# Kernel optimization log

Measured on AMD Instinct MI355X. Metric: run time of the kernel, lower is better.

## Reference

```python
import jax, jax.numpy as jnp
import numpy as np
import math

H = 256      # hidden_dim
L = 2        # num_layers
K = 30       # prediction_length
TD = 32      # time_encoding_dim
DT = 0.1


def _time_encodings():
    # (K, TD): sinusoidal PE over TD-1 dims + normalized time ratio, per _get_time_encoding
    pos = jnp.arange(K, dtype=jnp.float32)[:, None]
    div = jnp.exp(jnp.arange(0, TD - 1, 2, dtype=jnp.float32) * (-math.log(10000.0) / (TD - 1)))
    pe = jnp.zeros((K, TD - 1), dtype=jnp.float32)
    pe = pe.at[:, 0::2].set(jnp.sin(pos * div))
    pe = pe.at[:, 1::2].set(jnp.cos(pos * div[: (TD - 1) // 2]))
    return jnp.concatenate([pe, pos / K], axis=1)


def _gru_cell(x, h, Wih, Whh, bih, bhh):
    # PyTorch GRU cell: r,z,n gate order
    gi = x @ Wih.T + bih
    gh = h @ Whh.T + bhh
    ir, iz, inn = jnp.split(gi, 3, axis=1)
    hr, hz, hn = jnp.split(gh, 3, axis=1)
    r = jax.nn.sigmoid(ir + hr)
    z = jax.nn.sigmoid(iz + hz)
    n = jnp.tanh(inn + r * hn)
    return (1.0 - z) * n + z * h


def setup_inputs() -> dict:
    key = jax.random.key(0)
    ks = jax.random.split(key, 16)
    B = 4096
    in0 = 3 + TD + H  # gru_input_size = 291
    s = 0.05
    p = lambda k, shp: jax.random.normal(k, shp, dtype=jnp.float32) * s
    return {
        'h_fused': jax.random.normal(ks[0], (B, H), dtype=jnp.float32),
        'initial_state': jax.random.normal(ks[1], (B, 3), dtype=jnp.float32),
        'W1': p(ks[2], (H, H)), 'b1': jnp.zeros((H,), jnp.float32),
        'W2': p(ks[3], (L * H, H)), 'b2': jnp.zeros((L * H,), jnp.float32),
        'Wih0': p(ks[4], (3 * H, in0)), 'Whh0': p(ks[5], (3 * H, H)),
        'bih0': jnp.zeros((3 * H,), jnp.float32), 'bhh0': jnp.zeros((3 * H,), jnp.float32),
        'Wih1': p(ks[6], (3 * H, H)), 'Whh1': p(ks[7], (3 * H, H)),
        'bih1': jnp.zeros((3 * H,), jnp.float32), 'bhh1': jnp.zeros((3 * H,), jnp.float32),
        'Wout': p(ks[8], (3, H)), 'bout': jnp.zeros((3,), jnp.float32),
    }


def reference(h_fused, initial_state, W1, b1, W2, b2,
              Wih0, Whh0, bih0, bhh0, Wih1, Whh1, bih1, bhh1, Wout, bout):
    B = h_fused.shape[0]
    # init_mlp: Linear -> ReLU -> Linear -> Tanh, reshape to per-layer hidden states
    h_init = jnp.tanh(jax.nn.relu(h_fused @ W1.T + b1) @ W2.T + b2)  # (B, L*H)
    h_layers = h_init.reshape(B, L, H).transpose(1, 0, 2)            # (L, B, H)
    te = _time_encodings()                                           # (K, TD)
    pos0 = jnp.repeat(initial_state[:, 0:1], 3, axis=1)              # position history window

    def step(carry, te_k):
        s_t, h0, h1, pos_hist = carry
        gin = jnp.concatenate([s_t, jnp.broadcast_to(te_k, (B, TD)), h_fused], axis=1)
        h0n = _gru_cell(gin, h0, Wih0, Whh0, bih0, bhh0)
        h1n = _gru_cell(h0n, h1, Wih1, Whh1, bih1, bhh1)
        qr = h1n @ Wout.T + bout                                     # (B, 3)
        q_lo = qr[:, 0]
        q_med = q_lo + jax.nn.softplus(qr[:, 1] - q_lo)
        q_hi = q_med + jax.nn.softplus(qr[:, 2] - q_med)
        x_next = q_med  # inference path (no teacher forcing)
        ph = jnp.concatenate([pos_hist[:, 1:], x_next[:, None]], axis=1)
        v = (ph[:, 2] - ph[:, 0]) / (2.0 * DT)                       # central-diff velocity
        a = (ph[:, 2] - 2.0 * ph[:, 1] + ph[:, 0]) / (DT * DT)       # second-diff accel
        s_next = jnp.stack([x_next, v, a], axis=1)
        return (s_next, h0n, h1n, ph), (q_lo, q_med, q_hi)

    _, (qlo, qmed, qhi) = jax.lax.scan(step, (initial_state, h_layers[0], h_layers[1], pos0), te)
    # scan stacks along step axis -> (K, B); transpose to (B, K)
    return (qlo.T, qmed.T, qhi.T)
```

## Files before the change

kernel.cpp:

```cpp
#include <hip/hip_runtime.h>

#define HDIM 256
#define KSTEPS 30
#define RPB 16
#define NTHR 512

typedef _Float16 f16x8 __attribute__((ext_vector_type(8)));
typedef float f32x4 __attribute__((ext_vector_type(4)));

__device__ __forceinline__ f32x4 mfma16(f16x8 a, f16x8 b, f32x4 c) {
  return __builtin_amdgcn_mfma_f32_16x16x32_f16(a, b, c, 0, 0, 0);
}

__device__ __forceinline__ float fsigm(float x) {
  return __builtin_amdgcn_rcpf(1.0f + __expf(-x));
}
__device__ __forceinline__ float ftanh(float x) {
  float t = __expf(2.0f * x);
  return 1.0f - 2.0f * __builtin_amdgcn_rcpf(t + 1.0f);
}
__device__ __forceinline__ float softplusf(float x) {
  return fmaxf(x, 0.0f) + log1pf(__expf(-fabsf(x)));
}

__device__ __forceinline__ int swz(int r, int c) {
  return r * 512 + ((c * 2) ^ ((r & 7) << 4));
}

__device__ __forceinline__ void wrsplit(char* hi, char* lo, int off, float v) {
  _Float16 h = (_Float16)v;
  *(_Float16*)(hi + off) = h;
  *(_Float16*)(lo + off) = (_Float16)(v - (float)h);
}
__device__ __forceinline__ float rdpair(const char* hi, const char* lo, int off) {
  return (float)*(const _Float16*)(hi + off) + (float)*(const _Float16*)(lo + off);
}

__device__ __forceinline__ void glds16(const _Float16* src, char* lds) {
  __builtin_amdgcn_global_load_lds(
      (const __attribute__((address_space(1))) unsigned int*)src,
      (__attribute__((address_space(3))) unsigned int*)lds, 16, 0, 0);
}

__device__ __forceinline__ void stage6(const _Float16* src, char* dst) {
  glds16(src,        dst);
  glds16(src + 512,  dst + 1024);
  glds16(src + 1024, dst + 2048);
  glds16(src + 1536, dst + 3072);
  glds16(src + 2048, dst + 4096);
  glds16(src + 2560, dst + 5120);
}

#define WAITV(n) do { asm volatile("s_waitcnt vmcnt(" #n ")"); \
  __builtin_amdgcn_sched_barrier(0); } while (0)

__global__ __launch_bounds__(256) void prep_kernel(
    const float* __restrict__ W1, const float* __restrict__ W2,
    const float* __restrict__ Wih0, const float* __restrict__ Whh0,
    const float* __restrict__ Wih1, const float* __restrict__ Whh1,
    const float* __restrict__ hf,
    _Float16* __restrict__ Whh0p, _Float16* __restrict__ Wih1p,
    _Float16* __restrict__ Whh1p,
    _Float16* __restrict__ W1h, _Float16* __restrict__ W1l,
    _Float16* __restrict__ W2h, _Float16* __restrict__ W2l,
    _Float16* __restrict__ Wih0hh, _Float16* __restrict__ Wih0hl,
    _Float16* __restrict__ hfh, _Float16* __restrict__ hfl,
    float* __restrict__ teW, int B)
{
  int e = blockIdx.x * 256 + threadIdx.x;
  if (e < 3*196608) {
    int m = e / 196608, p = e % 196608;
    int j = p & 7;
    int lane = (p >> 3) & 63;
    int c = lane & 15, ks = lane >> 4;
    int fi = (p >> 9) % 6;
    int wt = p / 3072;
    int t = wt & 7, wv = wt >> 3;
    int ct = fi / 3, g = fi % 3;
    int row = wv*32 + ct*16 + c + g*256;
    int col = t*32 + ks*8 + j;
    const float* src = (m == 0) ? Whh0 : (m == 1) ? Wih1 : Whh1;
    _Float16* dst = (m == 0) ? Whh0p : (m == 1) ? Wih1p : Whh1p;
    dst[p] = (_Float16)src[row*256 + col];
    return;
  } e -= 3*196608;
  if (e < 65536)  { float x = W1[e]; _Float16 h = (_Float16)x; W1h[e] = h; W1l[e] = (_Float16)(x - (float)h); return; } e -= 65536;
  if (e < 131072) { float x = W2[e]; _Float16 h = (_Float16)x; W2h[e] = h; W2l[e] = (_Float16)(x - (float)h); return; } e -= 131072;
  if (e < 196608) { int n = e >> 8, c = e & 255; float x = Wih0[n*291 + 35 + c]; _Float16 h = (_Float16)x; Wih0hh[e] = h; Wih0hl[e] = (_Float16)(x - (float)h); return; } e -= 196608;
  if (e < B*HDIM) { float x = hf[e]; _Float16 h = (_Float16)x; hfh[e] = h; hfl[e] = (_Float16)(x - (float)h); return; } e -= B*HDIM;
  if (e < KSTEPS*768) {
    int k = e / 768, n = e % 768;
    float pos = (float)k;
    const float fac = -9.210340371976184f / 31.0f;
    float acc = 0.0f;
    #pragma unroll
    for (int j = 0; j < 31; ++j) {
      int i = j >> 1;
      float ang = pos * expf((float)(2*i) * fac);
      float t = (j & 1) ? cosf(ang) : sinf(ang);
      acc += t * Wih0[n*291 + 3 + j];
    }
    acc += (pos / 30.0f) * Wih0[n*291 + 3 + 31];
    teW[e] = acc;
  }
}

__global__ __launch_bounds__(64) void xc_kernel(
    const _Float16* __restrict__ hfh, const _Float16* __restrict__ hfl,
    const _Float16* __restrict__ Wh, const _Float16* __restrict__ Wl,
    const float* __restrict__ bih0, float* __restrict__ XcT, int B)
{
  int l = threadIdx.x, l15 = l & 15, l4 = l >> 4;
  int bm = blockIdx.x;
  int bn = blockIdx.y;
  f32x4 acc[4];
  #pragma unroll
  for (int i = 0; i < 4; ++i) acc[i] = (f32x4){0,0,0,0};
  const _Float16* ah = hfh + (size_t)(bm*16 + l15)*256 + l4*8;
  const _Float16* al = hfl + (size_t)(bm*16 + l15)*256 + l4*8;
  #pragma unroll
  for (int kk = 0; kk < 8; ++kk) {
    f16x8 aH = *(const f16x8*)(ah + kk*32);
    f16x8 aL = *(const f16x8*)(al + kk*32);
    #pragma unroll
    for (int i = 0; i < 4; ++i) {
      size_t boff = (size_t)(bn*64 + i*16 + l15)*256 + l4*8 + kk*32;
      f16x8 bH = *(const f16x8*)(Wh + boff);
      f16x8 bL = *(const f16x8*)(Wl + boff);
      acc[i] = mfma16(aH, bH, acc[i]);
      acc[i] = mfma16(aL, bH, acc[i]);
      acc[i] = mfma16(aH, bL, acc[i]);
    }
  }
  #pragma unroll
  for (int i = 0; i < 4; ++i) {
    int n = bn*64 + i*16 + l15;
    float bb = bih0[n];
    #pragma unroll
    for (int j = 0; j < 4; ++j) {
      int r = bm*16 + l4*4 + j;
      XcT[(size_t)n*B + r] = acc[i][j] + bb;
    }
  }
}

#define OFF_H0H   0
#define OFF_H0L   8192
#define OFF_H1H   16384
#define OFF_H1L   24576
#define OFF_SLAB  32768
#define OFF_WS3   131072
#define OFF_BHH0  140288
#define OFF_BI1   143360
#define OFF_BH1   146432
#define OFF_WOUT  149504
#define OFF_SPH   152576
#define OFF_BOUT  153088
#define LDS_BYTES 153104

__global__ __launch_bounds__(NTHR) void gru_main(
    const float* __restrict__ istate,
    const float* __restrict__ b1g, const float* __restrict__ b2g,
    const float* __restrict__ Wih0, const float* __restrict__ bhh0g,
    const float* __restrict__ bih1g, const float* __restrict__ bhh1g,
    const float* __restrict__ Woutg, const float* __restrict__ boutg,
    const _Float16* __restrict__ Whh0p, const _Float16* __restrict__ Wih1p,
    const _Float16* __restrict__ Whh1p,
    const _Float16* __restrict__ W1h, const _Float16* __restrict__ W1l,
    const _Float16* __restrict__ W2h, const _Float16* __restrict__ W2l,
    const _Float16* __restrict__ hfh, const _Float16* __restrict__ hfl,
    const float* __restrict__ teW, const float* __restrict__ XcT,
    float* __restrict__ out, int B)
{
  extern __shared__ char smem[];
  char* h0H = smem + OFF_H0H;  char* h0L = smem + OFF_H0L;
  char* h1H = smem + OFF_H1H;  char* h1L = smem + OFF_H1L;
  float* Ws3   = (float*)(smem + OFF_WS3);
  float* bhh0L = (float*)(smem + OFF_BHH0);
  float* bi1L  = (float*)(smem + OFF_BI1);
  float* bh1L  = (float*)(smem + OFF_BH1);
  float* WoutL = (float*)(smem + OFF_WOUT);
  float* sph   = (float*)(smem + OFF_SPH);
  float* boutL = (float*)(smem + OFF_BOUT);

  const int tid = threadIdx.x;
  const int w = tid >> 6;
  const int lane = tid & 63;
  const int l15 = lane & 15;
  const int l4 = lane >> 4;
  const int row0 = blockIdx.x * RPB;

  const int wsb = __builtin_amdgcn_readfirstlane(OFF_SLAB + w * 6144);
  char* sl0 = smem + wsb;
  char* sl1 = sl0 + 49152;

  const _Float16* wpB  = Whh0p + (size_t)w*24576 + lane*8;
  const _Float16* wpH1 = Whh1p + (size_t)w*24576 + lane*8;
  const _Float16* wpI1 = Wih1p + (size_t)w*24576 + lane*8;

  for (int i = tid; i < 2304; i += NTHR) Ws3[i] = Wih0[(i/3)*291 + (i%3)];
  for (int i = tid; i < 768; i += NTHR) {
    bhh0L[i] = bhh0g[i]; bi1L[i] = bih1g[i]; bh1L[i] = bhh1g[i]; WoutL[i] = Woutg[i];
  }
  if (tid < 3) boutL[tid] = boutg[tid];
  if (tid < RPB) {
    const float* is = istate + (size_t)(row0 + tid) * 3;
    float s0 = is[0], s1 = is[1], s2 = is[2];
    float* sp = sph + tid*8;
    sp[0] = s0; sp[1] = s1; sp[2] = s2;
    sp[3] = s0; sp[4] = s0; sp[5] = s0;
  }

  {
    char* mH = smem + OFF_SLAB;
    char* mL = smem + OFF_SLAB + 8192;
    #pragma unroll
    for (int i = 0; i < 2; ++i) {
      int nt = w*2 + i;
      f32x4 acc0 = {0,0,0,0};
      const _Float16* brh = W1h + (nt*16 + l15)*256 + l4*8;
      const _Float16* brl = W1l + (nt*16 + l15)*256 + l4*8;
      const _Float16* a0h = hfh + (size_t)(row0 + l15)*256 + l4*8;
      const _Float16* a0l = hfl + (size_t)(row0 + l15)*256 + l4*8;
      #pragma unroll
      for (int kk = 0; kk < 8; ++kk) {
        f16x8 bH = *(const f16x8*)(brh + kk*32);
        f16x8 bL = *(const f16x8*)(brl + kk*32);
        f16x8 aH0 = *(const f16x8*)(a0h + kk*32);
        f16x8 aL0 = *(const f16x8*)(a0l + kk*32);
        acc0 = mfma16(aH0, bH, acc0); acc0 = mfma16(aL0, bH, acc0); acc0 = mfma16(aH0, bL, acc0);
      }
      int n = nt*16 + l15;
      float bb = b1g[n];
      #pragma unroll
      for (int j = 0; j < 4; ++j) {
        int r = l4*4 + j;
        float v = fmaxf(acc0[j] + bb, 0.0f);
        wrsplit(mH, mL, swz(r, n), v);
      }
    }
  }
  __syncthreads();

  {
    const char* mH = smem + OFF_SLAB;
    const char* mL = smem + OFF_SLAB + 8192;
    #pragma unroll
    for (int i = 0; i < 4; ++i) {
      int nt = w*4 + i;
      f32x4 acc0 = {0,0,0,0};
      const _Float16* brh = W2h + (nt*16 + l15)*256 + l4*8;
      const _Float16* brl = W2l + (nt*16 + l15)*256 + l4*8;
      #pragma unroll
      for (int kk = 0; kk < 8; ++kk) {
        int kc = kk*32 + l4*8;
        f16x8 bH = *(const f16x8*)(brh + kk*32);
        f16x8 bL = *(const f16x8*)(brl + kk*32);
        f16x8 aH0 = *(const f16x8*)(mH + swz(l15, kc));
        f16x8 aL0 = *(const f16x8*)(mL + swz(l15, kc));
        acc0 = mfma16(aH0, bH, acc0); acc0 = mfma16(aL0, bH, acc0); acc0 = mfma16(aH0, bL, acc0);
      }
      int n = nt*16 + l15;
      float bb = b2g[n];
      #pragma unroll
      for (int j = 0; j < 4; ++j) {
        int r = l4*4 + j;
        float v = ftanh(acc0[j] + bb);
        if (n < 256) wrsplit(h0H, h0L, swz(r, n), v);
        else         wrsplit(h1H, h1L, swz(r, n - 256), v);
      }
    }
  }
  __syncthreads();

  const size_t outP = (size_t)B * KSTEPS;
  const int boff = lane * 16;
  const int n0 = w*32 + l15;
  const int n1 = n0 + 16;

  stage6(wpB, sl0);

  for (int k = 0; k < KSTEPS; ++k) {
    const float* teWk = teW + k*768;

    f32x4 cR0 = {0,0,0,0}, cZ0 = {0,0,0,0}, cN0 = {0,0,0,0};
    f32x4 cR1 = {0,0,0,0}, cZ1 = {0,0,0,0}, cN1 = {0,0,0,0};
    #define GBODY(buf, t, AH, AL, r0, z0, nn0, r1, z1, nn1) do {      \
      f16x8 b0 = *(const f16x8*)((buf) + boff);                       \
      f16x8 b1 = *(const f16x8*)((buf) + 1024 + boff);                \
      f16x8 b2 = *(const f16x8*)((buf) + 2048 + boff);                \
      f16x8 b3 = *(const f16x8*)((buf) + 3072 + boff);                \
      f16x8 b4 = *(const f16x8*)((buf) + 4096 + boff);                \
      f16x8 b5 = *(const f16x8*)((buf) + 5120 + boff);                \
      int aoff = swz(l15, (t)*32 + l4*8);                             \
      f16x8 aH = *(const f16x8*)((AH) + aoff);                        \
      f16x8 aL = *(const f16x8*)((AL) + aoff);                        \
      r0  = mfma16(aH, b0, r0);  r0  = mfma16(aL, b0, r0);            \
      z0  = mfma16(aH, b1, z0);  z0  = mfma16(aL, b1, z0);            \
      nn0 = mfma16(aH, b2, nn0); nn0 = mfma16(aL, b2, nn0);           \
      r1  = mfma16(aH, b3, r1);  r1  = mfma16(aL, b3, r1);            \
      z1  = mfma16(aH, b4, z1);  z1  = mfma16(aL, b4, z1);            \
      nn1 = mfma16(aH, b5, nn1); nn1 = mfma16(aL, b5, nn1);           \
    } while (0)
    {
      char *cur = sl0, *nxt = sl1;
      for (int t = 0; t < 8; ++t) {
        const _Float16* nsrc = (t < 7) ? (wpB + (t+1)*3072) : wpH1;
        stage6(nsrc, nxt);
        WAITV(6);
        GBODY(cur, t, h0H, h0L, cR0, cZ0, cN0, cR1, cZ1, cN1);
        char* tmp = cur; cur = nxt; nxt = tmp;
      }
    }
    __syncthreads();

    #define EPI0(n, accR, accZ, accN) do {                                      \
      size_t base = (size_t)row0 + l4*4;                                        \
      f32x4 xcR = *(const f32x4*)(XcT + (size_t)(n)*B + base);                  \
      f32x4 xcZ = *(const f32x4*)(XcT + (size_t)(256 + (n))*B + base);          \
      f32x4 xcN = *(const f32x4*)(XcT + (size_t)(512 + (n))*B + base);          \
      float teR = teWk[n], teZ = teWk[256 + (n)], teN = teWk[512 + (n)];        \
      float wR0 = Ws3[(n)*3+0],       wR1 = Ws3[(n)*3+1],       wR2 = Ws3[(n)*3+2];          \
      float wZ0 = Ws3[((n)+256)*3+0], wZ1 = Ws3[((n)+256)*3+1], wZ2 = Ws3[((n)+256)*3+2];    \
      float wN0 = Ws3[((n)+512)*3+0], wN1 = Ws3[((n)+512)*3+1], wN2 = Ws3[((n)+512)*3+2];    \
      float bhR = bhh0L[n], bhZ = bhh0L[256 + (n)], bhN = bhh0L[512 + (n)];     \
      _Pragma("unroll")                                                         \
      for (int j = 0; j < 4; ++j) {                                             \
        int r = l4*4 + j;                                                       \
        const float* sp = sph + r*8;                                            \
        float s0 = sp[0], s1 = sp[1], s2 = sp[2];                               \
        float giR = xcR[j] + teR + s0*wR0 + s1*wR1 + s2*wR2;                    \
        float giZ = xcZ[j] + teZ + s0*wZ0 + s1*wZ1 + s2*wZ2;                    \
        float giN = xcN[j] + teN + s0*wN0 + s1*wN1 + s2*wN2;                    \
        float rg = fsigm(giR + accR[j] + bhR);                                  \
        float zg = fsigm(giZ + accZ[j] + bhZ);                                  \
        float ng = ftanh(giN + rg * (accN[j] + bhN));                           \
        float hold = rdpair(h0H, h0L, swz(r, n));                               \
        float hnew = (1.0f - zg) * ng + zg * hold;                              \
        wrsplit(h0H, h0L, swz(r, n), hnew);                                     \
      }                                                                         \
    } while (0)
    EPI0(n0, cR0, cZ0, cN0);
    EPI0(n1, cR1, cZ1, cN1);
    #undef EPI0
    __syncthreads();

    f32x4 aR0 = {0,0,0,0}, aZ0 = {0,0,0,0}, hN0 = {0,0,0,0}, iN0 = {0,0,0,0};
    f32x4 aR1 = {0,0,0,0}, aZ1 = {0,0,0,0}, hN1 = {0,0,0,0}, iN1 = {0,0,0,0};
    {
      char *cur = sl0, *nxt = sl1;
      for (int t = 0; t < 8; ++t) {
        const _Float16* nsrc = (t < 7) ? (wpH1 + (t+1)*3072) : wpI1;
        stage6(nsrc, nxt);
        WAITV(6);
        GBODY(cur, t, h1H, h1L, aR0, aZ0, hN0, aR1, aZ1, hN1);
        char* tmp = cur; cur = nxt; nxt = tmp;
      }
      for (int t = 0; t < 8; ++t) {
        const _Float16* nsrc = (t < 7) ? (wpI1 + (t+1)*3072) : wpB;
        stage6(nsrc, nxt);
        WAITV(6);
        GBODY(cur, t, h0H, h0L, aR0, aZ0, iN0, aR1, aZ1, iN1);
        char* tmp = cur; cur = nxt; nxt = tmp;
      }
    }
    #undef GBODY
    __syncthreads();

    #define EPI1(n, accR, accZ, accHN, accIN) do {                              \
      float biR = bi1L[n], biZ = bi1L[256+(n)], biN = bi1L[512+(n)];            \
      float bhRb = bh1L[n], bhZb = bh1L[256+(n)], bhNb = bh1L[512+(n)];         \
      _Pragma("unroll")                                                         \
      for (int j = 0; j < 4; ++j) {                                             \
        int r = l4*4 + j;                                                       \
        float rg = fsigm(accR[j] + biR + bhRb);                                 \
        float zg = fsigm(accZ[j] + biZ + bhZb);                                 \
        float ng = ftanh(accIN[j] + biN + rg * (accHN[j] + bhNb));              \
        float hold = rdpair(h1H, h1L, swz(r, n));                               \
        float hnew = (1.0f - zg) * ng + zg * hold;                              \
        wrsplit(h1H, h1L, swz(r, n), hnew);                                     \
      }                                                                         \
    } while (0)
    EPI1(n0, aR0, aZ0, hN0, iN0);
    EPI1(n1, aR1, aZ1, hN1, iN1);
    #undef EPI1
    __syncthreads();

    {
      int r = tid >> 5, li = tid & 31;
      float q0 = 0.0f, q1 = 0.0f, q2 = 0.0f;
      #pragma unroll
      for (int i = 0; i < 8; ++i) {
        int h = li + i*32;
        float v = rdpair(h1H, h1L, swz(r, h));
        q0 += v * WoutL[h];
        q1 += v * WoutL[256 + h];
        q2 += v * WoutL[512 + h];
      }
      #pragma unroll
      for (int m = 1; m < 32; m <<= 1) {
        q0 += __shfl_xor(q0, m);
        q1 += __shfl_xor(q1, m);
        q2 += __shfl_xor(q2, m);
      }
      if (li == 0) {
        float qlo = q0 + boutL[0];
        float qm  = qlo + softplusf(q1 + boutL[1] - qlo);
        float qhi = qm  + softplusf(q2 + boutL[2] - qm);
        size_t b = row0 + r;
        out[b*KSTEPS + k]            = qlo;
        out[outP + b*KSTEPS + k]     = qm;
        out[2*outP + b*KSTEPS + k]   = qhi;
        float* sp = sph + r*8;
        float p1 = sp[4], p2 = sp[5];
        sp[0] = qm;
        sp[1] = (qm - p1) * 5.0f;
        sp[2] = (qm - 2.0f*p2 + p1) * 100.0f;
        sp[3] = p1; sp[4] = p2; sp[5] = qm;
      }
    }
  }
}

extern "C" void kernel_launch(void* const* d_in, const int* in_sizes, int n_in,
                              void* d_out, int out_size, void* d_ws, size_t ws_size,
                              hipStream_t stream) {
  const float* hf     = (const float*)d_in[0];
  const float* istate = (const float*)d_in[1];
  const float* W1     = (const float*)d_in[2];
  const float* b1     = (const float*)d_in[3];
  const float* W2     = (const float*)d_in[4];
  const float* b2     = (const float*)d_in[5];
  const float* Wih0   = (const float*)d_in[6];
  const float* Whh0   = (const float*)d_in[7];
  const float* bih0   = (const float*)d_in[8];
  const float* bhh0   = (const float*)d_in[9];
  const float* Wih1   = (const float*)d_in[10];
  const float* Whh1   = (const float*)d_in[11];
  const float* bih1   = (const float*)d_in[12];
  const float* bhh1   = (const float*)d_in[13];
  const float* Wout   = (const float*)d_in[14];
  const float* bout   = (const float*)d_in[15];
  float* out = (float*)d_out;
  const int B = in_sizes[0] / HDIM;

  char* ws = (char*)d_ws;
  size_t o = 0;
  _Float16* Whh0p  = (_Float16*)(ws + o); o += 393216;
  _Float16* Wih1p  = (_Float16*)(ws + o); o += 393216;
  _Float16* Whh1p  = (_Float16*)(ws + o); o += 393216;
  _Float16* W1h    = (_Float16*)(ws + o); o += 131072;
  _Float16* W1l    = (_Float16*)(ws + o); o += 131072;
  _Float16* W2h    = (_Float16*)(ws + o); o += 262144;
  _Float16* W2l    = (_Float16*)(ws + o); o += 262144;
  _Float16* Wih0hh = (_Float16*)(ws + o); o += 393216;
  _Float16* Wih0hl = (_Float16*)(ws + o); o += 393216;
  _Float16* hfh    = (_Float16*)(ws + o); o += (size_t)B * HDIM * 2;
  _Float16* hfl    = (_Float16*)(ws + o); o += (size_t)B * HDIM * 2;
  float*    teW    = (float*)(ws + o);    o += (size_t)KSTEPS * 768 * 4;
  float*    XcT    = (float*)(ws + o);    o += (size_t)B * 768 * 4;
  if (ws_size < o) return;

  const int prep_total = 196608*3 + 65536 + 131072 + 196608 + B*HDIM + KSTEPS*768;
  prep_kernel<<<dim3((prep_total + 255) / 256), dim3(256), 0, stream>>>(
      W1, W2, Wih0, Whh0, Wih1, Whh1, hf,
      Whh0p, Wih1p, Whh1p, W1h, W1l, W2h, W2l, Wih0hh, Wih0hl, hfh, hfl, teW, B);

  xc_kernel<<<dim3(B/16, 12), dim3(64), 0, stream>>>(hfh, hfl, Wih0hh, Wih0hl, bih0, XcT, B);

  hipFuncSetAttribute((const void*)gru_main,
                      hipFuncAttributeMaxDynamicSharedMemorySize, LDS_BYTES);
  gru_main<<<dim3(B/RPB), dim3(NTHR), LDS_BYTES, stream>>>(
      istate, b1, b2, Wih0, bhh0, bih1, bhh1, Wout, bout,
      Whh0p, Wih1p, Whh1p, W1h, W1l, W2h, W2l, hfh, hfl, teW, XcT, out, B);
}
```

Before: 539.1 us.

## Double block threads so each wave owns one 16-column gate tile

Raises the block from 8 to 16 waves, giving each wave a single 16-column slice of the r/z/n gates instead of two. The prepacked weight layout, per-wave LDS staging slabs, staging size and the init MLP loops are all halved to match. The goal is more waves in flight to hide the serial recurrence's latency and to cut per-wave MFMA and epilogue work. In exchange there is more barrier overhead per step and higher register and LDS pressure per CU, which may lower occupancy.

```diff
diff --git a/kernel.cpp b/kernel.cpp
--- a/kernel.cpp
+++ b/kernel.cpp
@@ -3,7 +3,7 @@
 #define HDIM 256
 #define KSTEPS 30
 #define RPB 16
-#define NTHR 512
+#define NTHR 1024
 
 typedef _Float16 f16x8 __attribute__((ext_vector_type(8)));
 typedef float f32x4 __attribute__((ext_vector_type(4)));
@@ -42,13 +42,10 @@
       (__attribute__((address_space(3))) unsigned int*)lds, 16, 0, 0);
 }
 
-__device__ __forceinline__ void stage6(const _Float16* src, char* dst) {
+__device__ __forceinline__ void stage3(const _Float16* src, char* dst) {
   glds16(src,        dst);
   glds16(src + 512,  dst + 1024);
   glds16(src + 1024, dst + 2048);
-  glds16(src + 1536, dst + 3072);
-  glds16(src + 2048, dst + 4096);
-  glds16(src + 2560, dst + 5120);
 }
 
 #define WAITV(n) do { asm volatile("s_waitcnt vmcnt(" #n ")"); \
@@ -73,11 +70,10 @@
     int j = p & 7;
     int lane = (p >> 3) & 63;
     int c = lane & 15, ks = lane >> 4;
-    int fi = (p >> 9) % 6;
-    int wt = p / 3072;
+    int g = (p >> 9) % 3;
+    int wt = p / 1536;
     int t = wt & 7, wv = wt >> 3;
-    int ct = fi / 3, g = fi % 3;
-    int row = wv*32 + ct*16 + c + g*256;
+    int row = wv*16 + c + g*256;
     int col = t*32 + ks*8 + j;
     const float* src = (m == 0) ? Whh0 : (m == 1) ? Wih1 : Whh1;
     _Float16* dst = (m == 0) ? Whh0p : (m == 1) ? Wih1p : Whh1p;
@@ -190,13 +186,13 @@
   const int l4 = lane >> 4;
   const int row0 = blockIdx.x * RPB;
 
-  const int wsb = __builtin_amdgcn_readfirstlane(OFF_SLAB + w * 6144);
+  const int wsb = __builtin_amdgcn_readfirstlane(OFF_SLAB + w * 3072);
   char* sl0 = smem + wsb;
   char* sl1 = sl0 + 49152;
 
-  const _Float16* wpB  = Whh0p + (size_t)w*24576 + lane*8;
-  const _Float16* wpH1 = Whh1p + (size_t)w*24576 + lane*8;
-  const _Float16* wpI1 = Wih1p + (size_t)w*24576 + lane*8;
+  const _Float16* wpB  = Whh0p + (size_t)w*12288 + lane*8;
+  const _Float16* wpH1 = Whh1p + (size_t)w*12288 + lane*8;
+  const _Float16* wpI1 = Wih1p + (size_t)w*12288 + lane*8;
 
   for (int i = tid; i < 2304; i += NTHR) Ws3[i] = Wih0[(i/3)*291 + (i%3)];
   for (int i = tid; i < 768; i += NTHR) {
@@ -214,30 +210,27 @@
   {
     char* mH = smem + OFF_SLAB;
     char* mL = smem + OFF_SLAB + 8192;
-    #pragma unroll
-    for (int i = 0; i < 2; ++i) {
-      int nt = w*2 + i;
-      f32x4 acc0 = {0,0,0,0};
-      const _Float16* brh = W1h + (nt*16 + l15)*256 + l4*8;
-      const _Float16* brl = W1l + (nt*16 + l15)*256 + l4*8;
-      const _Float16* a0h = hfh + (size_t)(row0 + l15)*256 + l4*8;
-      const _Float16* a0l = hfl + (size_t)(row0 + l15)*256 + l4*8;
-      #pragma unroll
-      for (int kk = 0; kk < 8; ++kk) {
-        f16x8 bH = *(const f16x8*)(brh + kk*32);
-        f16x8 bL = *(const f16x8*)(brl + kk*32);
-        f16x8 aH0 = *(const f16x8*)(a0h + kk*32);
-        f16x8 aL0 = *(const f16x8*)(a0l + kk*32);
-        acc0 = mfma16(aH0, bH, acc0); acc0 = mfma16(aL0, bH, acc0); acc0 = mfma16(aH0, bL, acc0);
-      }
-      int n = nt*16 + l15;
-      float bb = b1g[n];
-      #pragma unroll
-      for (int j = 0; j < 4; ++j) {
-        int r = l4*4 + j;
-        float v = fmaxf(acc0[j] + bb, 0.0f);
-        wrsplit(mH, mL, swz(r, n), v);
-      }
+    int nt = w;
+    f32x4 acc0 = {0,0,0,0};
+    const _Float16* brh = W1h + (nt*16 + l15)*256 + l4*8;
+    const _Float16* brl = W1l + (nt*16 + l15)*256 + l4*8;
+    const _Float16* a0h = hfh + (size_t)(row0 + l15)*256 + l4*8;
+    const _Float16* a0l = hfl + (size_t)(row0 + l15)*256 + l4*8;
+    #pragma unroll
+    for (int kk = 0; kk < 8; ++kk) {
+      f16x8 bH = *(const f16x8*)(brh + kk*32);
+      f16x8 bL = *(const f16x8*)(brl + kk*32);
+      f16x8 aH0 = *(const f16x8*)(a0h + kk*32);
+      f16x8 aL0 = *(const f16x8*)(a0l + kk*32);
+      acc0 = mfma16(aH0, bH, acc0); acc0 = mfma16(aL0, bH, acc0); acc0 = mfma16(aH0, bL, acc0);
+    }
+    int n = nt*16 + l15;
+    float bb = b1g[n];
+    #pragma unroll
+    for (int j = 0; j < 4; ++j) {
+      int r = l4*4 + j;
+      float v = fmaxf(acc0[j] + bb, 0.0f);
+      wrsplit(mH, mL, swz(r, n), v);
     }
   }
   __syncthreads();
@@ -246,8 +239,8 @@
     const char* mH = smem + OFF_SLAB;
     const char* mL = smem + OFF_SLAB + 8192;
     #pragma unroll
-    for (int i = 0; i < 4; ++i) {
-      int nt = w*4 + i;
+    for (int i = 0; i < 2; ++i) {
+      int nt = w*2 + i;
       f32x4 acc0 = {0,0,0,0};
       const _Float16* brh = W2h + (nt*16 + l15)*256 + l4*8;
       const _Float16* brl = W2l + (nt*16 + l15)*256 + l4*8;
@@ -275,130 +268,115 @@
 
   const size_t outP = (size_t)B * KSTEPS;
   const int boff = lane * 16;
-  const int n0 = w*32 + l15;
-  const int n1 = n0 + 16;
-
-  stage6(wpB, sl0);
+  const int n0 = w*16 + l15;
+
+  stage3(wpB, sl0);
 
   for (int k = 0; k < KSTEPS; ++k) {
     const float* teWk = teW + k*768;
 
-    f32x4 cR0 = {0,0,0,0}, cZ0 = {0,0,0,0}, cN0 = {0,0,0,0};
-    f32x4 cR1 = {0,0,0,0}, cZ1 = {0,0,0,0}, cN1 = {0,0,0,0};
-    #define GBODY(buf, t, AH, AL, r0, z0, nn0, r1, z1, nn1) do {      \
+    f32x4 cR = {0,0,0,0}, cZ = {0,0,0,0}, cN = {0,0,0,0};
+    #define GBODY(buf, t, AH, AL, rr, zz, nn) do {                    \
       f16x8 b0 = *(const f16x8*)((buf) + boff);                       \
       f16x8 b1 = *(const f16x8*)((buf) + 1024 + boff);                \
       f16x8 b2 = *(const f16x8*)((buf) + 2048 + boff);                \
-      f16x8 b3 = *(const f16x8*)((buf) + 3072 + boff);                \
-      f16x8 b4 = *(const f16x8*)((buf) + 4096 + boff);                \
-      f16x8 b5 = *(const f16x8*)((buf) + 5120 + boff);                \
       int aoff = swz(l15, (t)*32 + l4*8);                             \
       f16x8 aH = *(const f16x8*)((AH) + aoff);                        \
       f16x8 aL = *(const f16x8*)((AL) + aoff);                        \
-      r0  = mfma16(aH, b0, r0);  r0  = mfma16(aL, b0, r0);            \
-      z0  = mfma16(aH, b1, z0);  z0  = mfma16(aL, b1, z0);            \
-      nn0 = mfma16(aH, b2, nn0); nn0 = mfma16(aL, b2, nn0);           \
-      r1  = mfma16(aH, b3, r1);  r1  = mfma16(aL, b3, r1);            \
-      z1  = mfma16(aH, b4, z1);  z1  = mfma16(aL, b4, z1);            \
-      nn1 = mfma16(aH, b5, nn1); nn1 = mfma16(aL, b5, nn1);           \
+      rr = mfma16(aH, b0, rr); rr = mfma16(aL, b0, rr);               \
+      zz = mfma16(aH, b1, zz); zz = mfma16(aL, b1, zz);               \
+      nn = mfma16(aH, b2, nn); nn = mfma16(aL, b2, nn);               \
     } while (0)
     {
       char *cur = sl0, *nxt = sl1;
       for (int t = 0; t < 8; ++t) {
-        const _Float16* nsrc = (t < 7) ? (wpB + (t+1)*3072) : wpH1;
-        stage6(nsrc, nxt);
-        WAITV(6);
-        GBODY(cur, t, h0H, h0L, cR0, cZ0, cN0, cR1, cZ1, cN1);
+        const _Float16* nsrc = (t < 7) ? (wpB + (t+1)*1536) : wpH1;
+        stage3(nsrc, nxt);
+        WAITV(3);
+        GBODY(cur, t, h0H, h0L, cR, cZ, cN);
         char* tmp = cur; cur = nxt; nxt = tmp;
       }
     }
     __syncthreads();
 
-    #define EPI0(n, accR, accZ, accN) do {                                      \
-      size_t base = (size_t)row0 + l4*4;                                        \
-      f32x4 xcR = *(const f32x4*)(XcT + (size_t)(n)*B + base);                  \
-      f32x4 xcZ = *(const f32x4*)(XcT + (size_t)(256 + (n))*B + base);          \
-      f32x4 xcN = *(const f32x4*)(XcT + (size_t)(512 + (n))*B + base);          \
-      float teR = teWk[n], teZ = teWk[256 + (n)], teN = teWk[512 + (n)];        \
-      float wR0 = Ws3[(n)*3+0],       wR1 = Ws3[(n)*3+1],       wR2 = Ws3[(n)*3+2];          \
-      float wZ0 = Ws3[((n)+256)*3+0], wZ1 = Ws3[((n)+256)*3+1], wZ2 = Ws3[((n)+256)*3+2];    \
-      float wN0 = Ws3[((n)+512)*3+0], wN1 = Ws3[((n)+512)*3+1], wN2 = Ws3[((n)+512)*3+2];    \
-      float bhR = bhh0L[n], bhZ = bhh0L[256 + (n)], bhN = bhh0L[512 + (n)];     \
-      _Pragma("unroll")                                                         \
-      for (int j = 0; j < 4; ++j) {                                             \
-        int r = l4*4 + j;                                                       \
-        const float* sp = sph + r*8;                                            \
-        float s0 = sp[0], s1 = sp[1], s2 = sp[2];                               \
-        float giR = xcR[j] + teR + s0*wR0 + s1*wR1 + s2*wR2;                    \
-        float giZ = xcZ[j] + teZ + s0*wZ0 + s1*wZ1 + s2*wZ2;                    \
-        float giN = xcN[j] + teN + s0*wN0 + s1*wN1 + s2*wN2;                    \
-        float rg = fsigm(giR + accR[j] + bhR);                                  \
-        float zg = fsigm(giZ + accZ[j] + bhZ);                                  \
-        float ng = ftanh(giN + rg * (accN[j] + bhN));                           \
-        float hold = rdpair(h0H, h0L, swz(r, n));                               \
-        float hnew = (1.0f - zg) * ng + zg * hold;                              \
-        wrsplit(h0H, h0L, swz(r, n), hnew);                                     \
-      }                                                                         \
-    } while (0)
-    EPI0(n0, cR0, cZ0, cN0);
-    EPI0(n1, cR1, cZ1, cN1);
-    #undef EPI0
+    {
+      size_t base = (size_t)row0 + l4*4;
+      f32x4 xcR = *(const f32x4*)(XcT + (size_t)n0*B + base);
+      f32x4 xcZ = *(const f32x4*)(XcT + (size_t)(256 + n0)*B + base);
+      f32x4 xcN = *(const f32x4*)(XcT + (size_t)(512 + n0)*B + base);
+      float teR = teWk[n0], teZ = teWk[256 + n0], teN = teWk[512 + n0];
+      float wR0 = Ws3[n0*3+0],       wR1 = Ws3[n0*3+1],       wR2 = Ws3[n0*3+2];
+      float wZ0 = Ws3[(n0+256)*3+0], wZ1 = Ws3[(n0+256)*3+1], wZ2 = Ws3[(n0+256)*3+2];
+      float wN0 = Ws3[(n0+512)*3+0], wN1 = Ws3[(n0+512)*3+1], wN2 = Ws3[(n0+512)*3+2];
+      float bhR = bhh0L[n0], bhZ = bhh0L[256 + n0], bhN = bhh0L[512 + n0];
+      #pragma unroll
+      for (int j = 0; j < 4; ++j) {
+        int r = l4*4 + j;
+        const float* sp = sph + r*8;
+        float s0 = sp[0], s1 = sp[1], s2 = sp[2];
+        float giR = xcR[j] + teR + s0*wR0 + s1*wR1 + s2*wR2;
+        float giZ = xcZ[j] + teZ + s0*wZ0 + s1*wZ1 + s2*wZ2;
+        float giN = xcN[j] + teN + s0*wN0 + s1*wN1 + s2*wN2;
+        float rg = fsigm(giR + cR[j] + bhR);
+        float zg = fsigm(giZ + cZ[j] + bhZ);
+        float ng = ftanh(giN + rg * (cN[j] + bhN));
+        float hold = rdpair(h0H, h0L, swz(r, n0));
+        float hnew = (1.0f - zg) * ng + zg * hold;
+        wrsplit(h0H, h0L, swz(r, n0), hnew);
+      }
+    }
     __syncthreads();
 
-    f32x4 aR0 = {0,0,0,0}, aZ0 = {0,0,0,0}, hN0 = {0,0,0,0}, iN0 = {0,0,0,0};
-    f32x4 aR1 = {0,0,0,0}, aZ1 = {0,0,0,0}, hN1 = {0,0,0,0}, iN1 = {0,0,0,0};
+    f32x4 aR = {0,0,0,0}, aZ = {0,0,0,0}, hN = {0,0,0,0}, iN = {0,0,0,0};
     {
       char *cur = sl0, *nxt = sl1;
       for (int t = 0; t < 8; ++t) {
-        const _Float16* nsrc = (t < 7) ? (wpH1 + (t+1)*3072) : wpI1;
-        stage6(nsrc, nxt);
-        WAITV(6);
-        GBODY(cur, t, h1H, h1L, aR0, aZ0, hN0, aR1, aZ1, hN1);
+        const _Float16* nsrc = (t < 7) ? (wpH1 + (t+1)*1536) : wpI1;
+        stage3(nsrc, nxt);
+        WAITV(3);
+        GBODY(cur, t, h1H, h1L, aR, aZ, hN);
         char* tmp = cur; cur = nxt; nxt = tmp;
       }
       for (int t = 0; t < 8; ++t) {
-        const _Float16* nsrc = (t < 7) ? (wpI1 + (t+1)*3072) : wpB;
-        stage6(nsrc, nxt);
-        WAITV(6);
-        GBODY(cur, t, h0H, h0L, aR0, aZ0, iN0, aR1, aZ1, iN1);
+        const _Float16* nsrc = (t < 7) ? (wpI1 + (t+1)*1536) : wpB;
+        stage3(nsrc, nxt);
+        WAITV(3);
+        GBODY(cur, t, h0H, h0L, aR, aZ, iN);
         char* tmp = cur; cur = nxt; nxt = tmp;
       }
     }
     #undef GBODY
     __syncthreads();
 
-    #define EPI1(n, accR, accZ, accHN, accIN) do {                              \
-      float biR = bi1L[n], biZ = bi1L[256+(n)], biN = bi1L[512+(n)];            \
-      float bhRb = bh1L[n], bhZb = bh1L[256+(n)], bhNb = bh1L[512+(n)];         \
-      _Pragma("unroll")                                                         \
-      for (int j = 0; j < 4; ++j) {                                             \
-        int r = l4*4 + j;                                                       \
-        float rg = fsigm(accR[j] + biR + bhRb);                                 \
-        float zg = fsigm(accZ[j] + biZ + bhZb);                                 \
-        float ng = ftanh(accIN[j] + biN + rg * (accHN[j] + bhNb));              \
-        float hold = rdpair(h1H, h1L, swz(r, n));                               \
-        float hnew = (1.0f - zg) * ng + zg * hold;                              \
-        wrsplit(h1H, h1L, swz(r, n), hnew);                                     \
-      }                                                                         \
-    } while (0)
-    EPI1(n0, aR0, aZ0, hN0, iN0);
-    EPI1(n1, aR1, aZ1, hN1, iN1);
-    #undef EPI1
+    {
+      float biR = bi1L[n0], biZ = bi1L[256+n0], biN = bi1L[512+n0];
+      float bhRb = bh1L[n0], bhZb = bh1L[256+n0], bhNb = bh1L[512+n0];
+      #pragma unroll
+      for (int j = 0; j < 4; ++j) {
+        int r = l4*4 + j;
+        float rg = fsigm(aR[j] + biR + bhRb);
+        float zg = fsigm(aZ[j] + biZ + bhZb);
+        float ng = ftanh(iN[j] + biN + rg * (hN[j] + bhNb));
+        float hold = rdpair(h1H, h1L, swz(r, n0));
+        float hnew = (1.0f - zg) * ng + zg * hold;
+        wrsplit(h1H, h1L, swz(r, n0), hnew);
+      }
+    }
     __syncthreads();
 
     {
-      int r = tid >> 5, li = tid & 31;
+      int r = tid >> 6, li = lane;
       float q0 = 0.0f, q1 = 0.0f, q2 = 0.0f;
       #pragma unroll
-      for (int i = 0; i < 8; ++i) {
-        int h = li + i*32;
+      for (int i = 0; i < 4; ++i) {
+        int h = li + i*64;
         float v = rdpair(h1H, h1L, swz(r, h));
         q0 += v * WoutL[h];
         q1 += v * WoutL[256 + h];
         q2 += v * WoutL[512 + h];
       }
       #pragma unroll
-      for (int m = 1; m < 32; m <<= 1) {
+      for (int m = 1; m < 64; m <<= 1) {
         q0 += __shfl_xor(q0, m);
         q1 += __shfl_xor(q1, m);
         q2 += __shfl_xor(q2, m);
```

Result: slower. 1.004 ms (+86.1%).

## Load recurrent GRU weights directly into registers instead of LDS double-buffered staging

Applied to the files above, without the earlier changes.

Drops the async global-to-LDS double-buffered staging of the per-step GRU weight slabs. Each pass now loads the B fragments straight into VGPRs with a one-step register prefetch, and the work is split into two half passes per gate group. This frees about 80KB of LDS, which could allow more blocks per CU, and removes the vmcnt waits and LDS reads. The cost is that global or L2 latency is hidden only by a shallow register prefetch, and the A fragments are now read from LDS twice.

```diff
diff --git a/kernel.cpp b/kernel.cpp
--- a/kernel.cpp
+++ b/kernel.cpp
@@ -35,24 +35,6 @@
 __device__ __forceinline__ float rdpair(const char* hi, const char* lo, int off) {
   return (float)*(const _Float16*)(hi + off) + (float)*(const _Float16*)(lo + off);
 }
-
-__device__ __forceinline__ void glds16(const _Float16* src, char* lds) {
-  __builtin_amdgcn_global_load_lds(
-      (const __attribute__((address_space(1))) unsigned int*)src,
-      (__attribute__((address_space(3))) unsigned int*)lds, 16, 0, 0);
-}
-
-__device__ __forceinline__ void stage6(const _Float16* src, char* dst) {
-  glds16(src,        dst);
-  glds16(src + 512,  dst + 1024);
-  glds16(src + 1024, dst + 2048);
-  glds16(src + 1536, dst + 3072);
-  glds16(src + 2048, dst + 4096);
-  glds16(src + 2560, dst + 5120);
-}
-
-#define WAITV(n) do { asm volatile("s_waitcnt vmcnt(" #n ")"); \
-  __builtin_amdgcn_sched_barrier(0); } while (0)
 
 __global__ __launch_bounds__(256) void prep_kernel(
     const float* __restrict__ W1, const float* __restrict__ W2,
@@ -148,15 +130,15 @@
 #define OFF_H0L   8192
 #define OFF_H1H   16384
 #define OFF_H1L   24576
-#define OFF_SLAB  32768
-#define OFF_WS3   131072
-#define OFF_BHH0  140288
-#define OFF_BI1   143360
-#define OFF_BH1   146432
-#define OFF_WOUT  149504
-#define OFF_SPH   152576
-#define OFF_BOUT  153088
-#define LDS_BYTES 153104
+#define OFF_TMP   32768
+#define OFF_WS3   49152
+#define OFF_BHH0  58368
+#define OFF_BI1   61440
+#define OFF_BH1   64512
+#define OFF_WOUT  67584
+#define OFF_SPH   70656
+#define OFF_BOUT  71168
+#define LDS_BYTES 71184
 
 __global__ __launch_bounds__(NTHR) void gru_main(
     const float* __restrict__ istate,
@@ -190,10 +172,6 @@
   const int l4 = lane >> 4;
   const int row0 = blockIdx.x * RPB;
 
-  const int wsb = __builtin_amdgcn_readfirstlane(OFF_SLAB + w * 6144);
-  char* sl0 = smem + wsb;
-  char* sl1 = sl0 + 49152;
-
   const _Float16* wpB  = Whh0p + (size_t)w*24576 + lane*8;
   const _Float16* wpH1 = Whh1p + (size_t)w*24576 + lane*8;
   const _Float16* wpI1 = Wih1p + (size_t)w*24576 + lane*8;
@@ -212,8 +190,8 @@
   }
 
   {
-    char* mH = smem + OFF_SLAB;
-    char* mL = smem + OFF_SLAB + 8192;
+    char* mH = smem + OFF_TMP;
+    char* mL = smem + OFF_TMP + 8192;
     #pragma unroll
     for (int i = 0; i < 2; ++i) {
       int nt = w*2 + i;
@@ -243,8 +221,8 @@
   __syncthreads();
 
   {
-    const char* mH = smem + OFF_SLAB;
-    const char* mL = smem + OFF_SLAB + 8192;
+    const char* mH = smem + OFF_TMP;
+    const char* mL = smem + OFF_TMP + 8192;
     #pragma unroll
     for (int i = 0; i < 4; ++i) {
       int nt = w*4 + i;
@@ -274,44 +252,36 @@
   __syncthreads();
 
   const size_t outP = (size_t)B * KSTEPS;
-  const int boff = lane * 16;
   const int n0 = w*32 + l15;
   const int n1 = n0 + 16;
 
-  stage6(wpB, sl0);
+  f16x8 wR = *(const f16x8*)(wpB);
+  f16x8 wZ = *(const f16x8*)(wpB + 512);
+  f16x8 wN = *(const f16x8*)(wpB + 1024);
 
   for (int k = 0; k < KSTEPS; ++k) {
     const float* teWk = teW + k*768;
 
+    #define GPASS(TB, AH, AL, rr, zz, nn, NEXTP) do {                 \
+      for (int t = 0; t < 8; ++t) {                                   \
+        const _Float16* np_ = (t < 7) ? ((TB) + (t+1)*3072) : (NEXTP);\
+        f16x8 nR = *(const f16x8*)(np_);                              \
+        f16x8 nZ = *(const f16x8*)(np_ + 512);                        \
+        f16x8 nN = *(const f16x8*)(np_ + 1024);                       \
+        int aoff = swz(l15, t*32 + l4*8);                             \
+        f16x8 aH = *(const f16x8*)((AH) + aoff);                      \
+        f16x8 aL = *(const f16x8*)((AL) + aoff);                      \
+        rr = mfma16(aH, wR, rr); rr = mfma16(aL, wR, rr);             \
+        zz = mfma16(aH, wZ, zz); zz = mfma16(aL, wZ, zz);             \
+        nn = mfma16(aH, wN, nn); nn = mfma16(aL, wN, nn);             \
+        wR = nR; wZ = nZ; wN = nN;                                    \
+      }                                                               \
+    } while (0)
+
     f32x4 cR0 = {0,0,0,0}, cZ0 = {0,0,0,0}, cN0 = {0,0,0,0};
     f32x4 cR1 = {0,0,0,0}, cZ1 = {0,0,0,0}, cN1 = {0,0,0,0};
-    #define GBODY(buf, t, AH, AL, r0, z0, nn0, r1, z1, nn1) do {      \
-      f16x8 b0 = *(const f16x8*)((buf) + boff);                       \
-      f16x8 b1 = *(const f16x8*)((buf) + 1024 + boff);                \
-      f16x8 b2 = *(const f16x8*)((buf) + 2048 + boff);                \
-      f16x8 b3 = *(const f16x8*)((buf) + 3072 + boff);                \
-      f16x8 b4 = *(const f16x8*)((buf) + 4096 + boff);                \
-      f16x8 b5 = *(const f16x8*)((buf) + 5120 + boff);                \
-      int aoff = swz(l15, (t)*32 + l4*8);                             \
-      f16x8 aH = *(const f16x8*)((AH) + aoff);                        \
-      f16x8 aL = *(const f16x8*)((AL) + aoff);                        \
-      r0  = mfma16(aH, b0, r0);  r0  = mfma16(aL, b0, r0);            \
-      z0  = mfma16(aH, b1, z0);  z0  = mfma16(aL, b1, z0);            \
-      nn0 = mfma16(aH, b2, nn0); nn0 = mfma16(aL, b2, nn0);           \
-      r1  = mfma16(aH, b3, r1);  r1  = mfma16(aL, b3, r1);            \
-      z1  = mfma16(aH, b4, z1);  z1  = mfma16(aL, b4, z1);            \
-      nn1 = mfma16(aH, b5, nn1); nn1 = mfma16(aL, b5, nn1);           \
-    } while (0)
-    {
-      char *cur = sl0, *nxt = sl1;
-      for (int t = 0; t < 8; ++t) {
-        const _Float16* nsrc = (t < 7) ? (wpB + (t+1)*3072) : wpH1;
-        stage6(nsrc, nxt);
-        WAITV(6);
-        GBODY(cur, t, h0H, h0L, cR0, cZ0, cN0, cR1, cZ1, cN1);
-        char* tmp = cur; cur = nxt; nxt = tmp;
-      }
-    }
+    GPASS(wpB,        h0H, h0L, cR0, cZ0, cN0, wpB + 1536);
+    GPASS(wpB + 1536, h0H, h0L, cR1, cZ1, cN1, wpH1);
     __syncthreads();
 
     #define EPI0(n, accR, accZ, accN) do {                                      \
@@ -347,24 +317,11 @@
 
     f32x4 aR0 = {0,0,0,0}, aZ0 = {0,0,0,0}, hN0 = {0,0,0,0}, iN0 = {0,0,0,0};
     f32x4 aR1 = {0,0,0,0}, aZ1 = {0,0,0,0}, hN1 = {0,0,0,0}, iN1 = {0,0,0,0};
-    {
-      char *cur = sl0, *nxt = sl1;
-      for (int t = 0; t < 8; ++t) {
-        const _Float16* nsrc = (t < 7) ? (wpH1 + (t+1)*3072) : wpI1;
-        stage6(nsrc, nxt);
-        WAITV(6);
-        GBODY(cur, t, h1H, h1L, aR0, aZ0, hN0, aR1, aZ1, hN1);
-        char* tmp = cur; cur = nxt; nxt = tmp;
-      }
-      for (int t = 0; t < 8; ++t) {
-        const _Float16* nsrc = (t < 7) ? (wpI1 + (t+1)*3072) : wpB;
-        stage6(nsrc, nxt);
-        WAITV(6);
-        GBODY(cur, t, h0H, h0L, aR0, aZ0, iN0, aR1, aZ1, iN1);
-        char* tmp = cur; cur = nxt; nxt = tmp;
-      }
-    }
-    #undef GBODY
+    GPASS(wpH1,        h1H, h1L, aR0, aZ0, hN0, wpH1 + 1536);
+    GPASS(wpH1 + 1536, h1H, h1L, aR1, aZ1, hN1, wpI1);
+    GPASS(wpI1,        h0H, h0L, aR0, aZ0, iN0, wpI1 + 1536);
+    GPASS(wpI1 + 1536, h0H, h0L, aR1, aZ1, iN1, wpB);
+    #undef GPASS
     __syncthreads();
 
     #define EPI1(n, accR, accZ, accHN, accIN) do {                              \
```

Result: slower. 1.735 ms (+221.9%).
